# Performance work log

Measured on AMD Instinct MI355X. Metric: run time of the kernel, lower is better.

The kernel has to match this reference:

```python
import jax, jax.numpy as jnp
import numpy as np
from math import sqrt

N_HEADS = 16

def _rope(t, freqs):
    # t: [b, n, l, hd]; freqs: [l, hd//2, 2] (real, imag of unit rotations)
    b, n, l, hd = t.shape
    t2 = t.reshape(b, n, l, hd // 2, 2)
    tr, ti = t2[..., 0], t2[..., 1]
    fr, fi = freqs[..., 0], freqs[..., 1]  # broadcast over b, n
    out_r = tr * fr - ti * fi
    out_i = tr * fi + ti * fr
    return jnp.stack([out_r, out_i], axis=-1).reshape(b, n, l, hd)

def setup_inputs() -> dict:
    key = jax.random.key(0)
    ks = jax.random.split(key, 6)
    B, L, D = 2, 2048, 1024
    HD = D // N_HEADS
    x = jax.random.normal(ks[0], (B, L, D), dtype=jnp.float32)
    # proper rotary frequencies: theta_i = 10000^{-2i/hd}, angle = pos * theta
    inv = 1.0 / (10000.0 ** (np.arange(0, HD, 2, dtype=np.float32) / HD))  # [HD//2]
    ang = np.arange(L, dtype=np.float32)[:, None] * inv[None, :]           # [L, HD//2]
    freqs = jnp.asarray(np.stack([np.cos(ang), np.sin(ang)], axis=-1))     # [L, HD//2, 2]
    # additive causal mask
    causal = jnp.tril(jnp.ones((L, L), dtype=bool))
    attention_mask = jnp.where(causal, 0.0, -1e9).astype(jnp.float32)[None, None]
    init = 1.0 / sqrt(D)
    Wq = jax.random.normal(ks[1], (D, D), dtype=jnp.float32) * init
    Wk = jax.random.normal(ks[2], (D, D), dtype=jnp.float32) * init
    Wv = jax.random.normal(ks[3], (D, D), dtype=jnp.float32) * init
    Wo = jax.random.normal(ks[4], (D, D), dtype=jnp.float32) * init
    return {"x": x, "freqs": freqs, "attention_mask": attention_mask,
            "Wq": Wq, "Wk": Wk, "Wv": Wv, "Wo": Wo}

def reference(x, freqs, attention_mask, Wq, Wk, Wv, Wo):
    b, l, d = x.shape
    n = N_HEADS
    hd = d // n
    scale = sqrt(hd)

    def split_heads(t):  # [b, l, d] -> [b, n, l, hd]
        return t.reshape(b, l, n, hd).transpose(0, 2, 1, 3)

    q = split_heads(x @ Wq.T)
    k = split_heads(x @ Wk.T)
    v = split_heads(x @ Wv.T)
    q = _rope(q, freqs)
    k = _rope(k, freqs)
    scores = jnp.einsum('bnqd,bnkd->bnqk', q, k) / scale
    attn = jax.nn.softmax(scores + attention_mask, axis=-1)
    out = jnp.einsum('bnqk,bnkd->bnqd', attn, v)
    out = out.transpose(0, 2, 1, 3).reshape(b, l, d)
    return out @ Wo.T
```

## Files before the change

### kernel.cpp

```cpp
#include <hip/hip_runtime.h>
#include <stdint.h>

#define LSEQ 2048
#define DMODEL 1024
#define NHEADS 16
#define HDIM 64
#define MROWS 4096

typedef __attribute__((ext_vector_type(8))) short short8;
typedef __attribute__((ext_vector_type(4))) float f32x4;
typedef __attribute__((ext_vector_type(16))) float f32x16;

static __device__ __forceinline__ unsigned short f2bf(float f) {
    unsigned u = __builtin_bit_cast(unsigned, f);
    u += 0x7fffu + ((u >> 16) & 1u);
    return (unsigned short)(u >> 16);
}
static __device__ __forceinline__ unsigned cvt_pk_bf16(float a, float b) {
    unsigned r;
    asm("v_cvt_pk_bf16_f32 %0, %1, %2" : "=v"(r) : "v"(a), "v"(b));
    return r;
}

static __device__ __forceinline__ void gl2lds16(const unsigned short* g, unsigned short* l) {
    __builtin_amdgcn_global_load_lds(
        (const __attribute__((address_space(1))) unsigned int*)g,
        (__attribute__((address_space(3))) unsigned int*)l, 16, 0, 0);
}

__global__ void cast_all(const float* __restrict__ x,  const float* __restrict__ Wq,
                         const float* __restrict__ Wk, const float* __restrict__ Wv,
                         const float* __restrict__ Wo,
                         unsigned short* __restrict__ xb,
                         unsigned short* __restrict__ wqkv,
                         unsigned short* __restrict__ wo) {
    int i = blockIdx.x * blockDim.x + threadIdx.x;
    const float4* src;
    ushort4* dst;
    if (i < 1048576) {
        src = (const float4*)x + i;
        dst = (ushort4*)xb + i;
    } else {
        int t = i - 1048576;
        int w = t >> 18;
        int j = t & 262143;
        const float* s = (w == 0) ? Wq : (w == 1) ? Wk : (w == 2) ? Wv : Wo;
        src = (const float4*)s + j;
        dst = (w == 3) ? ((ushort4*)wo + j) : ((ushort4*)wqkv + (size_t)w * 262144 + j);
    }
    float4 v = *src;
    ushort4 o;
    o.x = f2bf(v.x); o.y = f2bf(v.y); o.z = f2bf(v.z); o.w = f2bf(v.w);
    *dst = o;
}

template <int TM, bool OUT_BF16>
__global__ __launch_bounds__(256) void gemm_nt(const unsigned short* __restrict__ A,
                                               const unsigned short* __restrict__ Bw,
                                               void* __restrict__ C,
                                               int Kdim, int ldc) {
    constexpr int WM = TM / 2;
    __shared__ unsigned short As[TM * 32];
    __shared__ unsigned short Bs[128 * 32];
    int tid = threadIdx.x;
    int lane = tid & 63, wave = tid >> 6;
    int row16 = lane & 15, quad = lane >> 4;
    int wm = wave & 1, wn = wave >> 1;
    int m0 = blockIdx.x * TM;
    int n0 = blockIdx.y * 128;

    int srow = wave * 16 + (lane >> 2);
    int scol = (lane & 3) * 8;
    const unsigned short* Ag = A  + (size_t)(m0 + srow) * Kdim + scol;
    const unsigned short* Bg = Bw + (size_t)(n0 + srow) * Kdim + scol;
    unsigned short* Asw = As + wave * 512;
    unsigned short* Bsw = Bs + wave * 512;

    f32x4 acc[WM / 16][4];
    #pragma unroll
    for (int i = 0; i < WM / 16; ++i)
        #pragma unroll
        for (int j = 0; j < 4; ++j) acc[i][j] = (f32x4){0.f, 0.f, 0.f, 0.f};

    for (int k0 = 0; k0 < Kdim; k0 += 32) {
        #pragma unroll
        for (int i = 0; i < TM / 64; ++i)
            gl2lds16(Ag + (size_t)i * 64 * Kdim + k0, Asw + i * 2048);
        gl2lds16(Bg + k0, Bsw);
        gl2lds16(Bg + (size_t)64 * Kdim + k0, Bsw + 2048);
        __syncthreads();

        short8 af[WM / 16], bf_[4];
        #pragma unroll
        for (int mi = 0; mi < WM / 16; ++mi)
            af[mi] = *(const short8*)(As + (wm * WM + mi * 16 + row16) * 32 + quad * 8);
        #pragma unroll
        for (int ni = 0; ni < 4; ++ni)
            bf_[ni] = *(const short8*)(Bs + (wn * 64 + ni * 16 + row16) * 32 + quad * 8);
        #pragma unroll
        for (int mi = 0; mi < WM / 16; ++mi)
            #pragma unroll
            for (int ni = 0; ni < 4; ++ni)
                acc[mi][ni] = __builtin_amdgcn_mfma_f32_16x16x32_bf16(af[mi], bf_[ni], acc[mi][ni], 0, 0, 0);
        __syncthreads();
    }

    int orow = m0 + wm * WM + quad * 4;
    int ocol = n0 + wn * 64 + row16;
    #pragma unroll
    for (int mi = 0; mi < WM / 16; ++mi)
        #pragma unroll
        for (int ni = 0; ni < 4; ++ni)
            #pragma unroll
            for (int r = 0; r < 4; ++r) {
                size_t idx = (size_t)(orow + mi * 16 + r) * ldc + (ocol + ni * 16);
                if (OUT_BF16) ((unsigned short*)C)[idx] = f2bf(acc[mi][ni][r]);
                else          ((float*)C)[idx]          = acc[mi][ni][r];
            }
}

#define QKV_PHASE(VN, T, DO_STAGE)                                          \
  {                                                                         \
    asm volatile("s_waitcnt vmcnt(" #VN ")" ::: "memory");                  \
    __builtin_amdgcn_s_barrier();                                           \
    __builtin_amdgcn_sched_barrier(0);                                      \
    if (DO_STAGE) {                                                         \
      int t3 = (T) + 3;                                                     \
      int ws = (t3 & 3) * 16384;                                            \
      const unsigned short* asrc = AgL + t3 * 32;                           \
      const unsigned short* bsrc = BgL + t3 * 32;                           \
      gl2lds16(asrc,                        lds + ws + stA);                \
      gl2lds16(asrc + (size_t)128 * DMODEL, lds + ws + stA + 4096);         \
      gl2lds16(bsrc,                        lds + ws + stB);                \
      gl2lds16(bsrc + (size_t)128 * DMODEL, lds + ws + stB + 4096);         \
    }                                                                       \
    {                                                                       \
      int rs = ((T) & 3) * 16384;                                           \
      const unsigned short* Ar = lds + rs + rdA;                            \
      const unsigned short* Br = lds + rs + 8192 + rdB;                     \
      short8 bfr[4];                                                        \
      _Pragma("unroll")                                                     \
      for (int j = 0; j < 4; ++j) bfr[j] = *(const short8*)(Br + j * 512);  \
      _Pragma("unroll")                                                     \
      for (int q = 0; q < 2; ++q) {                                         \
        short8 af[4];                                                       \
        _Pragma("unroll")                                                   \
        for (int i = 0; i < 4; ++i)                                         \
          af[i] = *(const short8*)(Ar + q * 2048 + i * 512);                \
        __builtin_amdgcn_s_setprio(1);                                      \
        _Pragma("unroll")                                                   \
        for (int i = 0; i < 4; ++i)                                         \
          _Pragma("unroll")                                                 \
          for (int j = 0; j < 4; ++j)                                       \
            acc[q * 4 + i][j] = __builtin_amdgcn_mfma_f32_16x16x32_bf16(    \
                af[i], bfr[j], acc[q * 4 + i][j], 0, 0, 0);                 \
        __builtin_amdgcn_s_setprio(0);                                      \
      }                                                                     \
    }                                                                       \
  }

__global__ __launch_bounds__(512, 2) void gemm_qkv(const unsigned short* __restrict__ A,
                                                   const unsigned short* __restrict__ Bw,
                                                   const float* __restrict__ freqs,
                                                   unsigned short* __restrict__ qh,
                                                   unsigned short* __restrict__ kh,
                                                   unsigned short* __restrict__ vt) {
    extern __shared__ unsigned short lds[];

    int tid  = threadIdx.x;
    int lane = tid & 63, wave = tid >> 6;
    int row16 = lane & 15, quad = lane >> 4;
    int wm = wave & 1, wn = wave >> 1;

    int id  = blockIdx.x;
    int gid = (id & 7) * 24 + (id >> 3);
    int bx = gid / 12, by = gid % 12;
    int m0 = bx * 256, n0 = by * 256;

    int off0 = tid * 16;
    int g = off0 ^ (((off0 >> 7) & 3) << 4);
    int srow = g >> 6;
    int scol = (g & 63) >> 1;
    const unsigned short* AgL = A  + (size_t)(m0 + srow) * DMODEL + scol;
    const unsigned short* BgL = Bw + (size_t)(n0 + srow) * DMODEL + scol;

    int stA = wave * 512;
    int stB = 8192 + wave * 512;

    int sw  = ((row16 >> 1) & 3) << 4;
    int rdA = ((((wm * 128 + row16) * 64) + quad * 16) ^ sw) >> 1;
    int rdB = ((((wn *  64 + row16) * 64) + quad * 16) ^ sw) >> 1;

    f32x4 acc[8][4];
    #pragma unroll
    for (int i = 0; i < 8; ++i)
        #pragma unroll
        for (int j = 0; j < 4; ++j) acc[i][j] = (f32x4){0.f, 0.f, 0.f, 0.f};

    #pragma unroll
    for (int p = 0; p < 3; ++p) {
        int ws = p * 16384;
        const unsigned short* asrc = AgL + p * 32;
        const unsigned short* bsrc = BgL + p * 32;
        gl2lds16(asrc,                        lds + ws + stA);
        gl2lds16(asrc + (size_t)128 * DMODEL, lds + ws + stA + 4096);
        gl2lds16(bsrc,                        lds + ws + stB);
        gl2lds16(bsrc + (size_t)128 * DMODEL, lds + ws + stB + 4096);
    }

    for (int t = 0; t < 30; ++t) {
        QKV_PHASE(8, t, (t < 29))
    }
    QKV_PHASE(4, 30, false)
    QKV_PHASE(0, 31, false)

    int region = n0 >> 10;
    int b = m0 >> 11;
    int orow0 = m0 + wm * 128 + quad * 4;
    int ocol0 = n0 + wn * 64 + row16;

    if (region < 2) {
        unsigned short* dst = region ? kh : qh;
        float sgn = (row16 & 1) ? 1.f : -1.f;
        #pragma unroll
        for (int nf = 0; nf < 4; ++nf) {
            int c = ocol0 - region * 1024 + nf * 16;
            int head = c >> 6, d = c & 63, ii = d >> 1;
            unsigned short* hb = dst + ((size_t)(b * NHEADS + head) * LSEQ) * HDIM + d;
            #pragma unroll
            for (int mf = 0; mf < 8; ++mf)
                #pragma unroll
                for (int r = 0; r < 4; ++r) {
                    int l = (orow0 + mf * 16 + r) & 2047;
                    float own = acc[mf][nf][r];
                    float par = __shfl_xor(own, 1);
                    float2 f = *(const float2*)(freqs + ((size_t)l * 32 + ii) * 2);
                    float out = own * f.x + par * (sgn * f.y);
                    hb[(size_t)l * HDIM] = f2bf(out);
                }
        }
    } else {
        #pragma unroll
        for (int nf = 0; nf < 4; ++nf) {
            int c = ocol0 - 2048 + nf * 16;
            int head = c >> 6, d = c & 63;
            size_t vbase = ((size_t)(b * NHEADS + head) * HDIM + d) * LSEQ;
            #pragma unroll
            for (int mf = 0; mf < 8; ++mf) {
                int l0 = (orow0 + mf * 16) & 2047;
                ushort4 o;
                o.x = f2bf(acc[mf][nf][0]);
                o.y = f2bf(acc[mf][nf][1]);
                o.z = f2bf(acc[mf][nf][2]);
                o.w = f2bf(acc[mf][nf][3]);
                *(ushort4*)(vt + vbase + l0) = o;
            }
        }
    }
}

__global__ __launch_bounds__(256, 4) void attn_flash(const unsigned short* __restrict__ qh,
                                                     const unsigned short* __restrict__ kh,
                                                     const unsigned short* __restrict__ vt,
                                                     unsigned short* __restrict__ oh) {
    __shared__ char smem[33280];
    unsigned short* ldsb = (unsigned short*)smem;
    float* mO = (float*)smem;
    float* mL = (float*)(smem + 16384);
    const float CS = 0.18033688011112042f;
    const float CB = 28.853900817779268f;

    int lane = threadIdx.x & 63;
    int wave = threadIdx.x >> 6;
    int l31 = lane & 31;
    int h   = lane >> 5;
    int kq  = wave >> 1, qq = wave & 1;

    int id  = blockIdx.x;
    int xcd = id & 7;
    int bn  = xcd * 4 + ((id >> 3) & 3);
    int s   = id >> 5;
    int u = s & 7, rnd = s >> 3;
    int qb = (rnd == 0) ? (31 - u) : (rnd == 1) ? (16 + u) : (rnd == 2) ? (15 - u) : u;
    int b = bn >> 4, n = bn & 15;

    const unsigned short* Qb = qh + (size_t)bn * LSEQ * HDIM;
    const unsigned short* Kb = kh + (size_t)bn * LSEQ * HDIM;
    const unsigned short* Vb = vt + (size_t)bn * HDIM * LSEQ;

    int q0 = qb * 64;
    int qabs = q0 + qq * 32 + l31;

    short8 qf[4];
    #pragma unroll
    for (int mf = 0; mf < 4; ++mf)
        qf[mf] = *(const short8*)(Qb + (size_t)(q0 + qq * 32 + l31) * HDIM + mf * 16 + h * 8);

    int sf  = wave >> 1;
    int m0s = (wave & 1) * 2;
    const unsigned short* kg = Kb + (size_t)(sf * 32 + l31) * HDIM + m0s * 16 + h * 8;
    const unsigned short* vg = Vb + (size_t)(sf * 32 + l31) * LSEQ + m0s * 16 + h * 8;
    int soff = (sf * 4 + m0s) * 512;

    f32x16 accO[2];
    #pragma unroll
    for (int i = 0; i < 16; ++i) { accO[0][i] = 0.f; accO[1][i] = 0.f; }
    float l_s = 0.f;

    int nk = qb + 1;

    auto stage = [&](int t) {
        int sl = (t & 1) * 4096;
        const unsigned short* kgk = kg + (size_t)t * 64 * HDIM;
        const unsigned short* vgk = vg + t * 64;
        gl2lds16(kgk,      ldsb + sl + soff);
        gl2lds16(kgk + 16, ldsb + sl + soff + 512);
        gl2lds16(vgk,      ldsb + 8192 + sl + soff);
        gl2lds16(vgk + 16, ldsb + 8192 + sl + soff + 512);
    };

    stage(0);
    stage(1);

    for (int kt = 0; kt < nk; ++kt) {
        if (kt < nk - 1) asm volatile("s_waitcnt vmcnt(4)" ::: "memory");
        else             asm volatile("s_waitcnt vmcnt(0)" ::: "memory");
        __builtin_amdgcn_s_barrier();
        __builtin_amdgcn_sched_barrier(0);

        int cb = (kt & 1) * 4096;
        const unsigned short* Kc = ldsb + cb;
        const unsigned short* Vc = ldsb + 8192 + cb;

        bool edge = (kt == nk - 1);
        bool dead = edge && (kq == 1) && (qq == 0);

        if (!dead) {
            f32x16 z;
            #pragma unroll
            for (int i = 0; i < 16; ++i) z[i] = 0.f;
            __builtin_amdgcn_s_setprio(1);
            #pragma unroll
            for (int m = 0; m < 4; ++m) {
                short8 kf = *(const short8*)(Kc + (kq * 4 + m) * 512 + lane * 8);
                z = __builtin_amdgcn_mfma_f32_32x32x16_bf16(kf, qf[m], z, 0, 0, 0);
            }
            __builtin_amdgcn_s_setprio(0);

            float p[16];
            bool maskz = edge && (kq == qq);
            #pragma unroll
            for (int r = 0; r < 16; ++r) {
                float e = __builtin_amdgcn_exp2f(z[r] * CS - CB);
                if (maskz) {
                    int kabs = kt * 64 + kq * 32 + (r & 3) + 8 * (r >> 2) + 4 * h;
                    if (kabs > qabs) e = 0.f;
                }
                p[r] = e;
            }
            float ps = 0.f;
            #pragma unroll
            for (int r = 0; r < 16; ++r) ps += p[r];
            l_s += ps;

            uint2 P4[4];
            #pragma unroll
            for (int g = 0; g < 4; ++g) {
                P4[g].x = cvt_pk_bf16(p[4 * g],     p[4 * g + 1]);
                P4[g].y = cvt_pk_bf16(p[4 * g + 2], p[4 * g + 3]);
            }
            short8 bfr[2];
            bool hb = (h != 0);
            #pragma unroll
            for (int m = 0; m < 2; ++m) {
                uint2 own = hb ? P4[1 + 2 * m] : P4[2 * m];
                uint2 snd = hb ? P4[2 * m]     : P4[1 + 2 * m];
                uint2 rcv;
                rcv.x = __shfl_xor(snd.x, 32);
                rcv.y = __shfl_xor(snd.y, 32);
                uint4 bb;
                bb.x = hb ? rcv.x : own.x;
                bb.y = hb ? rcv.y : own.y;
                bb.z = hb ? own.x : rcv.x;
                bb.w = hb ? own.y : rcv.y;
                bfr[m] = __builtin_bit_cast(short8, bb);
            }

            __builtin_amdgcn_s_setprio(1);
            #pragma unroll
            for (int dq = 0; dq < 2; ++dq)
                #pragma unroll
                for (int m = 0; m < 2; ++m) {
                    short8 vf = *(const short8*)(Vc + (dq * 4 + kq * 2 + m) * 512 + lane * 8);
                    accO[dq] = __builtin_amdgcn_mfma_f32_32x32x16_bf16(vf, bfr[m], accO[dq], 0, 0, 0);
                }
            __builtin_amdgcn_s_setprio(0);
        }

        __builtin_amdgcn_sched_barrier(0);
        __builtin_amdgcn_s_barrier();
        if (kt + 2 < nk) stage(kt + 2);
    }

    l_s += __shfl_xor(l_s, 32);

    if (kq == 1) {
        #pragma unroll
        for (int dq = 0; dq < 2; ++dq)
            #pragma unroll
            for (int r = 0; r < 16; ++r)
                mO[(qq * 2 + dq) * 1024 + r * 64 + lane] = accO[dq][r];
        mL[qq * 64 + lane] = l_s;
    }
    __syncthreads();
    if (kq == 0) {
        float inv = 1.0f / (l_s + mL[qq * 64 + lane]);
        #pragma unroll
        for (int dq = 0; dq < 2; ++dq)
            #pragma unroll
            for (int g = 0; g < 4; ++g) {
                float o0 = (accO[dq][4 * g]     + mO[(qq * 2 + dq) * 1024 + (4 * g)     * 64 + lane]) * inv;
                float o1 = (accO[dq][4 * g + 1] + mO[(qq * 2 + dq) * 1024 + (4 * g + 1) * 64 + lane]) * inv;
                float o2 = (accO[dq][4 * g + 2] + mO[(qq * 2 + dq) * 1024 + (4 * g + 2) * 64 + lane]) * inv;
                float o3 = (accO[dq][4 * g + 3] + mO[(qq * 2 + dq) * 1024 + (4 * g + 3) * 64 + lane]) * inv;
                ushort4 o;
                o.x = f2bf(o0); o.y = f2bf(o1); o.z = f2bf(o2); o.w = f2bf(o3);
                int d = dq * 32 + 8 * g + 4 * h;
                *(ushort4*)(oh + (size_t)(b * LSEQ + q0 + qq * 32 + l31) * DMODEL + n * HDIM + d) = o;
            }
    }
}

extern "C" void kernel_launch(void* const* d_in, const int* in_sizes, int n_in,
                              void* d_out, int out_size, void* d_ws, size_t ws_size,
                              hipStream_t stream) {
    const float* x     = (const float*)d_in[0];
    const float* freqs = (const float*)d_in[1];
    const float* Wq = (const float*)d_in[3];
    const float* Wk = (const float*)d_in[4];
    const float* Wv = (const float*)d_in[5];
    const float* Wo = (const float*)d_in[6];

    char* ws = (char*)d_ws;
    unsigned short* xb   = (unsigned short*)ws; ws += (size_t)MROWS * DMODEL * 2;
    unsigned short* wqkv = (unsigned short*)ws; ws += (size_t)3 * DMODEL * DMODEL * 2;
    unsigned short* wo   = (unsigned short*)ws; ws += (size_t)DMODEL * DMODEL * 2;
    unsigned short* qh   = (unsigned short*)ws; ws += (size_t)32 * LSEQ * HDIM * 2;
    unsigned short* kh   = (unsigned short*)ws; ws += (size_t)32 * LSEQ * HDIM * 2;
    unsigned short* vt   = (unsigned short*)ws; ws += (size_t)32 * HDIM * LSEQ * 2;
    unsigned short* oh   = (unsigned short*)ws; ws += (size_t)MROWS * DMODEL * 2;

    static bool attr_set = false;
    if (!attr_set) {
        (void)hipFuncSetAttribute((const void*)gemm_qkv,
                                  hipFuncAttributeMaxDynamicSharedMemorySize, 131072);
        attr_set = true;
    }

    cast_all<<<8192, 256, 0, stream>>>(x, Wq, Wk, Wv, Wo, xb, wqkv, wo);

    gemm_qkv<<<192, 512, 131072, stream>>>(xb, wqkv, freqs, qh, kh, vt);

    attn_flash<<<1024, 256, 0, stream>>>(qh, kh, vt, oh);

    gemm_nt<64, false><<<dim3(MROWS / 64, DMODEL / 128), 256, 0, stream>>>(oh, wo, (float*)d_out, DMODEL, DMODEL);
}
```

Baseline: 196.6 us.

## Restructure QKV GEMM mainloop into double-buffered 64-wide K tiles with interleaved phases

Replaces the 4-stage ring of 32-wide K slices in the QKV projection GEMM with a 2-buffer scheme holding 64-wide K tiles. Each tile is split into four sub-phases that interleave LDS fragment reads, global-to-LDS staging of the next tile, and MFMA blocks, with barriers around each compute block. The aim is to hide global loads and LDS reads behind MFMA work in a ping-pong style schedule. The cost is twice as many barriers per K step and a shallower prefetch depth than the old three-tile lookahead.

```diff
diff --git a/kernel.cpp b/kernel.cpp
--- a/kernel.cpp
+++ b/kernel.cpp
@@ -119,44 +119,42 @@
             }
 }
 
-#define QKV_PHASE(VN, T, DO_STAGE)                                          \
-  {                                                                         \
-    asm volatile("s_waitcnt vmcnt(" #VN ")" ::: "memory");                  \
-    __builtin_amdgcn_s_barrier();                                           \
-    __builtin_amdgcn_sched_barrier(0);                                      \
-    if (DO_STAGE) {                                                         \
-      int t3 = (T) + 3;                                                     \
-      int ws = (t3 & 3) * 16384;                                            \
-      const unsigned short* asrc = AgL + t3 * 32;                           \
-      const unsigned short* bsrc = BgL + t3 * 32;                           \
-      gl2lds16(asrc,                        lds + ws + stA);                \
-      gl2lds16(asrc + (size_t)128 * DMODEL, lds + ws + stA + 4096);         \
-      gl2lds16(bsrc,                        lds + ws + stB);                \
-      gl2lds16(bsrc + (size_t)128 * DMODEL, lds + ws + stB + 4096);         \
-    }                                                                       \
-    {                                                                       \
-      int rs = ((T) & 3) * 16384;                                           \
-      const unsigned short* Ar = lds + rs + rdA;                            \
-      const unsigned short* Br = lds + rs + 8192 + rdB;                     \
-      short8 bfr[4];                                                        \
-      _Pragma("unroll")                                                     \
-      for (int j = 0; j < 4; ++j) bfr[j] = *(const short8*)(Br + j * 512);  \
-      _Pragma("unroll")                                                     \
-      for (int q = 0; q < 2; ++q) {                                         \
-        short8 af[4];                                                       \
-        _Pragma("unroll")                                                   \
-        for (int i = 0; i < 4; ++i)                                         \
-          af[i] = *(const short8*)(Ar + q * 2048 + i * 512);                \
-        __builtin_amdgcn_s_setprio(1);                                      \
-        _Pragma("unroll")                                                   \
-        for (int i = 0; i < 4; ++i)                                         \
-          _Pragma("unroll")                                                 \
-          for (int j = 0; j < 4; ++j)                                       \
-            acc[q * 4 + i][j] = __builtin_amdgcn_mfma_f32_16x16x32_bf16(    \
-                af[i], bfr[j], acc[q * 4 + i][j], 0, 0, 0);                 \
-        __builtin_amdgcn_s_setprio(0);                                      \
-      }                                                                     \
-    }                                                                       \
+
+#define VM_NOP
+#define VM_W4 asm volatile("s_waitcnt vmcnt(4)" ::: "memory");
+#define VM_W0 asm volatile("s_waitcnt vmcnt(0)" ::: "memory");
+
+#define QKV_PH(KK, MH, DO_STAGE, LDST, GSRC, VMW)                            \
+  {                                                                          \
+    if ((MH) == 0) {                                                         \
+      const unsigned short* Bp = lds + rs + 16384 + (KK) * 8192 + boff;      \
+      _Pragma("unroll")                                                      \
+      for (int j = 0; j < 4; ++j) bfr[j] = *(const short8*)(Bp + j * 512);   \
+    }                                                                        \
+    short8 af[4];                                                            \
+    {                                                                        \
+      const unsigned short* Ap = lds + rs + (KK) * 8192 + aoff + (MH) * 2048;\
+      _Pragma("unroll")                                                      \
+      for (int i = 0; i < 4; ++i) af[i] = *(const short8*)(Ap + i * 512);    \
+    }                                                                        \
+    if (DO_STAGE) {                                                          \
+      const unsigned short* gp = (GSRC);                                     \
+      gl2lds16(gp,          lds + (LDST) + wave * 512);                      \
+      gl2lds16(gp + 131072, lds + (LDST) + 4096 + wave * 512);               \
+    }                                                                        \
+    VMW                                                                      \
+    __builtin_amdgcn_sched_barrier(0);                                       \
+    __builtin_amdgcn_s_barrier();                                            \
+    __builtin_amdgcn_sched_barrier(0);                                       \
+    __builtin_amdgcn_s_setprio(1);                                           \
+    _Pragma("unroll")                                                        \
+    for (int i = 0; i < 4; ++i)                                              \
+      _Pragma("unroll")                                                      \
+      for (int j = 0; j < 4; ++j)                                            \
+        acc[(MH) * 4 + i][j] = __builtin_amdgcn_mfma_f32_16x16x32_bf16(      \
+            af[i], bfr[j], acc[(MH) * 4 + i][j], 0, 0, 0);                   \
+    __builtin_amdgcn_s_setprio(0);                                           \
+    __builtin_amdgcn_s_barrier();                                            \
   }
 
 __global__ __launch_bounds__(512, 2) void gemm_qkv(const unsigned short* __restrict__ A,
@@ -184,12 +182,9 @@
     const unsigned short* AgL = A  + (size_t)(m0 + srow) * DMODEL + scol;
     const unsigned short* BgL = Bw + (size_t)(n0 + srow) * DMODEL + scol;
 
-    int stA = wave * 512;
-    int stB = 8192 + wave * 512;
-
-    int sw  = ((row16 >> 1) & 3) << 4;
-    int rdA = ((((wm * 128 + row16) * 64) + quad * 16) ^ sw) >> 1;
-    int rdB = ((((wn *  64 + row16) * 64) + quad * 16) ^ sw) >> 1;
+    int sw   = ((row16 >> 1) & 3) << 4;
+    int aoff = (wm * 128 + row16) * 32 + (((quad * 16) ^ sw) >> 1);
+    int boff = (wn *  64 + row16) * 32 + (((quad * 16) ^ sw) >> 1);
 
     f32x4 acc[8][4];
     #pragma unroll
@@ -197,22 +192,35 @@
         #pragma unroll
         for (int j = 0; j < 4; ++j) acc[i][j] = (f32x4){0.f, 0.f, 0.f, 0.f};
 
-    #pragma unroll
-    for (int p = 0; p < 3; ++p) {
-        int ws = p * 16384;
-        const unsigned short* asrc = AgL + p * 32;
-        const unsigned short* bsrc = BgL + p * 32;
-        gl2lds16(asrc,                        lds + ws + stA);
-        gl2lds16(asrc + (size_t)128 * DMODEL, lds + ws + stA + 4096);
-        gl2lds16(bsrc,                        lds + ws + stB);
-        gl2lds16(bsrc + (size_t)128 * DMODEL, lds + ws + stB + 4096);
-    }
-
-    for (int t = 0; t < 30; ++t) {
-        QKV_PHASE(8, t, (t < 29))
-    }
-    QKV_PHASE(4, 30, false)
-    QKV_PHASE(0, 31, false)
+    gl2lds16(AgL,                lds + 0     + wave * 512);
+    gl2lds16(AgL + 131072,       lds + 4096  + wave * 512);
+    gl2lds16(BgL,                lds + 16384 + wave * 512);
+    gl2lds16(BgL + 131072,       lds + 20480 + wave * 512);
+    gl2lds16(AgL + 32,           lds + 8192  + wave * 512);
+    gl2lds16(AgL + 32 + 131072,  lds + 12288 + wave * 512);
+    gl2lds16(BgL + 32,           lds + 24576 + wave * 512);
+    gl2lds16(BgL + 32 + 131072,  lds + 28672 + wave * 512);
+    asm volatile("s_waitcnt vmcnt(4)" ::: "memory");
+    __builtin_amdgcn_s_barrier();
+
+    short8 bfr[4];
+    for (int t = 0; t < 15; ++t) {
+        const int rs = (t & 1) * 32768;
+        const int ws = ((t + 1) & 1) * 32768;
+        const unsigned short* An = AgL + (t + 1) * 64;
+        const unsigned short* Bn = BgL + (t + 1) * 64;
+        QKV_PH(0, 0, true, ws + 0,     An,      VM_NOP)
+        QKV_PH(0, 1, true, ws + 16384, Bn,      VM_W4)
+        QKV_PH(1, 0, true, ws + 8192,  An + 32, VM_NOP)
+        QKV_PH(1, 1, true, ws + 24576, Bn + 32, VM_W4)
+    }
+    {
+        const int rs = 32768;
+        QKV_PH(0, 0, false, 0, AgL, VM_NOP)
+        QKV_PH(0, 1, false, 0, AgL, VM_W0)
+        QKV_PH(1, 0, false, 0, AgL, VM_NOP)
+        QKV_PH(1, 1, false, 0, AgL, VM_NOP)
+    }
 
     int region = n0 >> 10;
     int b = m0 >> 11;
```

Measured after the change: 197.8 us. About the same (+0.6%).
